# Optimization experiments

Hardware: AMD Instinct MI355X
Metric: run time of the kernel (lower is better)

The kernel has to match this reference:

```python
import jax, jax.numpy as jnp
from jax import lax
import numpy as np

B, T, C = 16, 2048, 1024
H, K = 16, 31
R = C // H
P = K - 1  # padding_l (causal)


def setup_inputs() -> dict:
    key = jax.random.key(0)
    kx, kw = jax.random.split(key)
    x = jax.random.normal(kx, (B, T, C), dtype=jnp.float32)
    # kaiming_uniform_(a=sqrt(5)) on (H, 1, K): fan_in = K, bound = 1/sqrt(K)
    bound = 1.0 / np.sqrt(K)
    weight = jax.random.uniform(kw, (H, 1, K), dtype=jnp.float32,
                                minval=-bound, maxval=bound)
    return {"x": x, "weight": weight}


def reference(x, weight):
    # weight_softmax=True: softmax over kernel dim (done in fp32, as in source)
    w = jax.nn.softmax(weight.reshape(H, K).astype(jnp.float32), axis=-1)
    w = w.astype(x.dtype)
    # Each head's kernel is shared across R = C//H channels -> depthwise kernel (C, 1, K)
    w_c = jnp.repeat(w, R, axis=0)            # (C, K)
    kernel = w_c[:, None, :]                  # (C, 1, K) in OIH layout
    x_t = jnp.transpose(x, (0, 2, 1))         # (B, C, T)
    # Cross-correlation with left pad P, right pad K-1-P (same math as the
    # banded-matrix _forward_expanded path / unfold1d + matmul)
    out = lax.conv_general_dilated(
        x_t, kernel,
        window_strides=(1,),
        padding=[(P, K - 1 - P)],
        feature_group_count=C,
        dimension_numbers=("NCH", "OIH", "NCH"),
    )                                         # (B, C, T)
    return jnp.transpose(out, (0, 2, 1))      # (B, T, C)
```

## Files before the change

### kernel.cpp

```cpp
#include <hip/hip_runtime.h>
#include <math.h>

#define TPB  512
#define KW   31
#define HALO (KW - 1)
#define TT   8
#define BT   128
#define RQ   40
constexpr int B_ = 16, T_ = 2048, C_ = 1024, H_ = 16;
constexpr int C2 = C_ / 2;
constexpr int PPH = 32;

__device__ inline float rfl(float v) {
    return __builtin_bit_cast(float, __builtin_amdgcn_readfirstlane(__builtin_bit_cast(int, v)));
}

__global__ __launch_bounds__(TPB, 8) void lconv_kernel(const float* __restrict__ x,
                                                       const float* __restrict__ w,
                                                       float* __restrict__ out) {
    __shared__ float smem[4 * RQ * 64];
    const int h   = blockIdx.x;
    const int b   = blockIdx.z;
    const int t0b = blockIdx.y * BT;
    const int tid  = threadIdx.x;
    const int lane = tid & 63;
    const int wid  = tid >> 6;

    const int qrow  = lane >> 4;
    const int chunk = lane & 15;
    const float* xh = x + (size_t)b * T_ * C_ + h * 64;
    #pragma unroll
    for (int q = wid; q < RQ; q += 8) {
        int t = t0b - HALO + 4 * q + qrow;
        t = min(max(t, 0), T_ - 1);
        const float* gsrc = xh + (size_t)t * C_ + chunk * 4;
        __builtin_amdgcn_global_load_lds(
            (const __attribute__((address_space(1))) uint32_t*)gsrc,
            (__attribute__((address_space(3))) uint32_t*)(smem + q * 256),
            16, 0, 0);
    }

    float wv[KW];
    {
        float v[KW];
        float m = -1e30f;
        #pragma unroll
        for (int k = 0; k < KW; ++k) { v[k] = w[h * KW + k]; m = fmaxf(m, v[k]); }
        float s = 0.f;
        #pragma unroll
        for (int k = 0; k < KW; ++k) { v[k] = __expf(v[k] - m); s += v[k]; }
        const float inv = 1.f / s;
        #pragma unroll
        for (int j = 0; j < KW; ++j) wv[j] = rfl(v[KW - 1 - j] * inv);
    }

    __syncthreads();
    if (blockIdx.y == 0) {
        for (int k = tid; k < HALO * 64; k += TPB) smem[k] = 0.f;
        __syncthreads();
    }

    const int pair = tid & 31;
    const int sub  = tid >> 5;

    float2 acc[TT];
    #pragma unroll
    for (int i = 0; i < TT; ++i) acc[i] = make_float2(0.f, 0.f);

    const float2* sm2 = (const float2*)smem;
    #pragma unroll
    for (int sr = 0; sr < TT + HALO; ++sr) {
        const float2 v = sm2[(size_t)(sub * TT + sr) * PPH + pair];
        const int ilo = (sr - HALO < 0) ? 0 : sr - HALO;
        const int ihi = (sr < TT - 1) ? sr : TT - 1;
        #pragma unroll
        for (int i = ilo; i <= ihi; ++i) {
            const float wj = wv[i + HALO - sr];
            acc[i].x = fmaf(wj, v.x, acc[i].x);
            acc[i].y = fmaf(wj, v.y, acc[i].y);
        }
    }

    float2* po = (float2*)out + ((size_t)b * T_ + t0b + sub * TT) * C2 + h * PPH + pair;
    #pragma unroll
    for (int i = 0; i < TT; ++i) po[(size_t)i * C2] = acc[i];
}

extern "C" void kernel_launch(void* const* d_in, const int* in_sizes, int n_in,
                              void* d_out, int out_size, void* d_ws, size_t ws_size,
                              hipStream_t stream) {
    const float* x = (const float*)d_in[0];
    const float* w = (const float*)d_in[1];
    float* out = (float*)d_out;

    dim3 grid(H_, T_ / BT, B_);
    hipLaunchKernelGGL(lconv_kernel, grid, dim3(TPB), 0, stream, x, w, out);
}
```

Baseline: 56.19 us.

## Make blocks persistent over eight time tiles with double-buffered async LDS loads

Each block now walks eight consecutive 128-step time tiles for one (batch, head). The next tile is prefetched into a second LDS buffer through global_load_lds while the current tile is computed, and the waits are tuned by hand with vmcnt. The grid shrinks to 512 blocks of 256 threads, and each thread computes 16 outputs instead of 8, which cuts the halo reloads per output. The left-edge padding now reads from a zeroed workspace buffer, set by an extra small launch, instead of being zeroed in shared memory. The trade-offs are less parallelism, which may leave CUs underused with only 512 blocks, more registers per thread, and a fragile hand-written vmcnt count.

```diff
diff --git a/kernel.cpp b/kernel.cpp
--- a/kernel.cpp
+++ b/kernel.cpp
@@ -1,49 +1,57 @@
 #include <hip/hip_runtime.h>
 #include <math.h>
 
-#define TPB  512
+#define TPB  256
 #define KW   31
-#define HALO (KW - 1)
-#define TT   8
+#define HALO 30
+#define TT   16
 #define BT   128
 #define RQ   40
+#define NT   8
 constexpr int B_ = 16, T_ = 2048, C_ = 1024, H_ = 16;
-constexpr int C2 = C_ / 2;
+constexpr int C2  = C_ / 2;
 constexpr int PPH = 32;
+
+__global__ void zerows_kernel(float* ws) { ws[threadIdx.x] = 0.f; }
 
 __device__ inline float rfl(float v) {
     return __builtin_bit_cast(float, __builtin_amdgcn_readfirstlane(__builtin_bit_cast(int, v)));
 }
 
-__global__ __launch_bounds__(TPB, 8) void lconv_kernel(const float* __restrict__ x,
-                                                       const float* __restrict__ w,
-                                                       float* __restrict__ out) {
-    __shared__ float smem[4 * RQ * 64];
-    const int h   = blockIdx.x;
-    const int b   = blockIdx.z;
-    const int t0b = blockIdx.y * BT;
+__global__ __launch_bounds__(TPB) void lconv_kernel(const float* __restrict__ x,
+                                                    const float* __restrict__ w,
+                                                    const float* __restrict__ zp,
+                                                    float* __restrict__ out) {
+    __shared__ float smem[2][RQ * 256];
+    const int bid = blockIdx.x;
+    const int h   = bid & 15;
+    const int b   = (bid >> 4) & 15;
+    const int yh  = bid >> 8;
     const int tid  = threadIdx.x;
-    const int lane = tid & 63;
-    const int wid  = tid >> 6;
+    const int lane = tid & 63, wid = tid >> 6;
+    const int qrow = lane >> 4, chunk = lane & 15;
+    const int pair = tid & 31,  sub = tid >> 5;
 
-    const int qrow  = lane >> 4;
-    const int chunk = lane & 15;
     const float* xh = x + (size_t)b * T_ * C_ + h * 64;
-    #pragma unroll
-    for (int q = wid; q < RQ; q += 8) {
-        int t = t0b - HALO + 4 * q + qrow;
-        t = min(max(t, 0), T_ - 1);
-        const float* gsrc = xh + (size_t)t * C_ + chunk * 4;
-        __builtin_amdgcn_global_load_lds(
-            (const __attribute__((address_space(1))) uint32_t*)gsrc,
-            (__attribute__((address_space(3))) uint32_t*)(smem + q * 256),
-            16, 0, 0);
-    }
 
+    auto stage = [&](const int buf, const int kt) {
+        const int t0b = (yh * NT + kt) * BT;
+        #pragma unroll
+        for (int q = wid; q < RQ; q += 4) {
+            const int t = t0b - HALO + 4 * q + qrow;
+            const float* src = (t < 0) ? (zp + chunk * 4)
+                                       : (xh + (size_t)min(t, T_ - 1) * C_ + chunk * 4);
+            __builtin_amdgcn_global_load_lds(
+                (const __attribute__((address_space(1))) uint32_t*)src,
+                (__attribute__((address_space(3))) uint32_t*)(&smem[buf][q * 256]),
+                16, 0, 0);
+        }
+    };
+
+    stage(0, 0);
     float wv[KW];
     {
-        float v[KW];
-        float m = -1e30f;
+        float v[KW]; float m = -1e30f;
         #pragma unroll
         for (int k = 0; k < KW; ++k) { v[k] = w[h * KW + k]; m = fmaxf(m, v[k]); }
         float s = 0.f;
@@ -53,37 +61,49 @@
         #pragma unroll
         for (int j = 0; j < KW; ++j) wv[j] = rfl(v[KW - 1 - j] * inv);
     }
+    asm volatile("s_waitcnt vmcnt(0) lgkmcnt(0)" ::: "memory");
+    __builtin_amdgcn_s_barrier();
+    __builtin_amdgcn_sched_barrier(0);
 
-    __syncthreads();
-    if (blockIdx.y == 0) {
-        for (int k = tid; k < HALO * 64; k += TPB) smem[k] = 0.f;
-        __syncthreads();
+    auto process = [&](const int buf, const int kt) {
+        if (kt + 1 < NT) stage(buf ^ 1, kt + 1);
+        __builtin_amdgcn_sched_barrier(0);
+
+        const int t0b = (yh * NT + kt) * BT;
+        float2 acc[TT];
+        #pragma unroll
+        for (int i = 0; i < TT; ++i) acc[i] = make_float2(0.f, 0.f);
+
+        const float2* sm2 = (const float2*)smem[buf];
+        #pragma unroll
+        for (int sr = 0; sr < TT + HALO; ++sr) {
+            const float2 v = sm2[(sub * TT + sr) * PPH + pair];
+            const int ilo = (sr - HALO < 0) ? 0 : sr - HALO;
+            const int ihi = (sr < TT - 1) ? sr : TT - 1;
+            #pragma unroll
+            for (int i = ilo; i <= ihi; ++i) {
+                const float wj = wv[i + HALO - sr];
+                acc[i].x = fmaf(wj, v.x, acc[i].x);
+                acc[i].y = fmaf(wj, v.y, acc[i].y);
+            }
+        }
+
+        float2* po = (float2*)out + ((size_t)b * T_ + t0b + sub * TT) * C2 + h * PPH + pair;
+        #pragma unroll
+        for (int i = 0; i < TT; ++i) po[(size_t)i * C2] = acc[i];
+
+        if (kt + 1 < NT) {
+            asm volatile("s_waitcnt vmcnt(16) lgkmcnt(0)" ::: "memory");
+            __builtin_amdgcn_s_barrier();
+            __builtin_amdgcn_sched_barrier(0);
+        }
+    };
+
+    #pragma unroll 1
+    for (int kp = 0; kp < NT / 2; ++kp) {
+        process(0, 2 * kp);
+        process(1, 2 * kp + 1);
     }
-
-    const int pair = tid & 31;
-    const int sub  = tid >> 5;
-
-    float2 acc[TT];
-    #pragma unroll
-    for (int i = 0; i < TT; ++i) acc[i] = make_float2(0.f, 0.f);
-
-    const float2* sm2 = (const float2*)smem;
-    #pragma unroll
-    for (int sr = 0; sr < TT + HALO; ++sr) {
-        const float2 v = sm2[(size_t)(sub * TT + sr) * PPH + pair];
-        const int ilo = (sr - HALO < 0) ? 0 : sr - HALO;
-        const int ihi = (sr < TT - 1) ? sr : TT - 1;
-        #pragma unroll
-        for (int i = ilo; i <= ihi; ++i) {
-            const float wj = wv[i + HALO - sr];
-            acc[i].x = fmaf(wj, v.x, acc[i].x);
-            acc[i].y = fmaf(wj, v.y, acc[i].y);
-        }
-    }
-
-    float2* po = (float2*)out + ((size_t)b * T_ + t0b + sub * TT) * C2 + h * PPH + pair;
-    #pragma unroll
-    for (int i = 0; i < TT; ++i) po[(size_t)i * C2] = acc[i];
 }
 
 extern "C" void kernel_launch(void* const* d_in, const int* in_sizes, int n_in,
@@ -92,7 +112,10 @@
     const float* x = (const float*)d_in[0];
     const float* w = (const float*)d_in[1];
     float* out = (float*)d_out;
+    float* zp  = (float*)d_ws;
 
-    dim3 grid(H_, T_ / BT, B_);
-    hipLaunchKernelGGL(lconv_kernel, grid, dim3(TPB), 0, stream, x, w, out);
+    hipLaunchKernelGGL(zerows_kernel, dim3(1), dim3(128), 0, stream, zp);
+
+    dim3 grid(512);
+    hipLaunchKernelGGL(lconv_kernel, grid, dim3(TPB), 0, stream, x, w, zp, out);
 }
```

Measured after the change: 56.47 us. About the same (+0.5%).

## Use 4-channel vector per thread with 256-thread blocks and nontemporal stores

Applied to the files above, without the earlier changes.

Halves the block size to 256 threads and has each thread compute four adjacent channels (float4) over 8 timesteps instead of two channels, so each LDS read feeds twice as many FMAs. The blockIdx.y==0 case now skips loads for negative timesteps instead of clamping them, and the LDS zeroing and async load completion share a single barrier. Outputs are written with nontemporal stores. The wider per-thread accumulators raise register pressure and the smaller blocks with no min-blocks hint may change occupancy. Skipping the negative-t loads relies on those LDS rows being zeroed before the barrier while async writes to other rows are still in flight.

```diff
diff --git a/kernel.cpp b/kernel.cpp
--- a/kernel.cpp
+++ b/kernel.cpp
@@ -1,49 +1,49 @@
 #include <hip/hip_runtime.h>
 #include <math.h>
 
-#define TPB  512
+#define TPB  256
 #define KW   31
-#define HALO (KW - 1)
+#define HALO 30
 #define TT   8
 #define BT   128
 #define RQ   40
 constexpr int B_ = 16, T_ = 2048, C_ = 1024, H_ = 16;
-constexpr int C2 = C_ / 2;
-constexpr int PPH = 32;
+constexpr int C4  = C_ / 4;
+constexpr int QPH = 16;
+
+typedef float f32x4 __attribute__((ext_vector_type(4)));
 
 __device__ inline float rfl(float v) {
     return __builtin_bit_cast(float, __builtin_amdgcn_readfirstlane(__builtin_bit_cast(int, v)));
 }
 
-__global__ __launch_bounds__(TPB, 8) void lconv_kernel(const float* __restrict__ x,
-                                                       const float* __restrict__ w,
-                                                       float* __restrict__ out) {
-    __shared__ float smem[4 * RQ * 64];
+__global__ __launch_bounds__(TPB) void lconv_kernel(const float* __restrict__ x,
+                                                    const float* __restrict__ w,
+                                                    float* __restrict__ out) {
+    __shared__ float smem[RQ * 256];
     const int h   = blockIdx.x;
     const int b   = blockIdx.z;
     const int t0b = blockIdx.y * BT;
     const int tid  = threadIdx.x;
-    const int lane = tid & 63;
-    const int wid  = tid >> 6;
+    const int lane = tid & 63, wid = tid >> 6;
+    const int qrow = lane >> 4, chunk = lane & 15;
 
-    const int qrow  = lane >> 4;
-    const int chunk = lane & 15;
     const float* xh = x + (size_t)b * T_ * C_ + h * 64;
     #pragma unroll
-    for (int q = wid; q < RQ; q += 8) {
-        int t = t0b - HALO + 4 * q + qrow;
-        t = min(max(t, 0), T_ - 1);
-        const float* gsrc = xh + (size_t)t * C_ + chunk * 4;
-        __builtin_amdgcn_global_load_lds(
-            (const __attribute__((address_space(1))) uint32_t*)gsrc,
-            (__attribute__((address_space(3))) uint32_t*)(smem + q * 256),
-            16, 0, 0);
+    for (int q = wid; q < RQ; q += 4) {
+        const int t = t0b - HALO + 4 * q + qrow;
+        if (t >= 0) {
+            const float* src = xh + (size_t)((t < T_ - 1) ? t : T_ - 1) * C_ + chunk * 4;
+            __builtin_amdgcn_global_load_lds(
+                (const __attribute__((address_space(1))) uint32_t*)src,
+                (__attribute__((address_space(3))) uint32_t*)(smem + q * 256),
+                16, 0, 0);
+        }
     }
 
     float wv[KW];
     {
-        float v[KW];
-        float m = -1e30f;
+        float v[KW]; float m = -1e30f;
         #pragma unroll
         for (int k = 0; k < KW; ++k) { v[k] = w[h * KW + k]; m = fmaxf(m, v[k]); }
         float s = 0.f;
@@ -54,36 +54,34 @@
         for (int j = 0; j < KW; ++j) wv[j] = rfl(v[KW - 1 - j] * inv);
     }
 
-    __syncthreads();
     if (blockIdx.y == 0) {
         for (int k = tid; k < HALO * 64; k += TPB) smem[k] = 0.f;
-        __syncthreads();
     }
+    __syncthreads();
 
-    const int pair = tid & 31;
-    const int sub  = tid >> 5;
+    const int quad = tid & 15;
+    const int sub  = tid >> 4;
 
-    float2 acc[TT];
+    f32x4 acc[TT];
     #pragma unroll
-    for (int i = 0; i < TT; ++i) acc[i] = make_float2(0.f, 0.f);
+    for (int i = 0; i < TT; ++i) acc[i] = (f32x4)0.f;
 
-    const float2* sm2 = (const float2*)smem;
+    const f32x4* sm4 = (const f32x4*)smem;
     #pragma unroll
     for (int sr = 0; sr < TT + HALO; ++sr) {
-        const float2 v = sm2[(size_t)(sub * TT + sr) * PPH + pair];
+        const f32x4 v = sm4[(sub * TT + sr) * QPH + quad];
         const int ilo = (sr - HALO < 0) ? 0 : sr - HALO;
         const int ihi = (sr < TT - 1) ? sr : TT - 1;
         #pragma unroll
         for (int i = ilo; i <= ihi; ++i) {
-            const float wj = wv[i + HALO - sr];
-            acc[i].x = fmaf(wj, v.x, acc[i].x);
-            acc[i].y = fmaf(wj, v.y, acc[i].y);
+            acc[i] += wv[i + HALO - sr] * v;
         }
     }
 
-    float2* po = (float2*)out + ((size_t)b * T_ + t0b + sub * TT) * C2 + h * PPH + pair;
+    f32x4* po = (f32x4*)out + ((size_t)b * T_ + t0b + sub * TT) * C4 + h * QPH + quad;
     #pragma unroll
-    for (int i = 0; i < TT; ++i) po[(size_t)i * C2] = acc[i];
+    for (int i = 0; i < TT; ++i)
+        __builtin_nontemporal_store(acc[i], po + (size_t)i * C4);
 }
 
 extern "C" void kernel_launch(void* const* d_in, const int* in_sizes, int n_in,
```

Result: faster. 46.70 us (-16.9%).
